# Optimization experiments

Hardware: AMD Instinct MI355X
Metric: run time of the kernel (lower is better)

The kernel has to match this reference:

```python
import jax, jax.numpy as jnp
import numpy as np

EMB = 768
HEADS = 12
DEPTH = EMB // HEADS
B, L = 8, 1024


def setup_inputs() -> dict:
    key = jax.random.key(0)
    ks = jax.random.split(key, 11)
    s = 1.0 / np.sqrt(EMB)
    inp = {
        "v": jax.random.normal(ks[0], (B, L, EMB), jnp.float32),
        "k": jax.random.normal(ks[1], (B, L, EMB), jnp.float32),
        "q": jax.random.normal(ks[2], (B, L, EMB), jnp.float32),
        # torch Linear weights: [out_features, in_features]
        "wq_w": jax.random.normal(ks[3], (EMB, EMB), jnp.float32) * s,
        "wq_b": jax.random.normal(ks[4], (EMB,), jnp.float32) * s,
        "wk_w": jax.random.normal(ks[5], (EMB, EMB), jnp.float32) * s,
        "wk_b": jax.random.normal(ks[6], (EMB,), jnp.float32) * s,
        "wv_w": jax.random.normal(ks[7], (EMB, EMB), jnp.float32) * s,
        "wv_b": jax.random.normal(ks[8], (EMB,), jnp.float32) * s,
        "dense_w": jax.random.normal(ks[9], (EMB, EMB), jnp.float32) * s,
        "dense_b": jax.random.normal(ks[10], (EMB,), jnp.float32) * s,
    }
    return inp


def _split_heads(x):
    b, l, _ = x.shape
    return x.reshape(b, l, HEADS, DEPTH).transpose(0, 2, 1, 3)  # [b,h,l,d]


def reference(v, k, q, wq_w, wq_b, wk_w, wk_b, wv_w, wv_b, dense_w, dense_b):
    qh = _split_heads(q @ wq_w.T + wq_b)
    kh = _split_heads(k @ wk_w.T + wk_b)
    vh = _split_heads(v @ wv_w.T + wv_b)
    # NOTE: module scales by sqrt(embedding_dim), not sqrt(depth)
    scale = 1.0 / jnp.sqrt(jnp.asarray(EMB, qh.dtype))
    score = jnp.einsum("bhqd,bhkd->bhqk", qh, kh) * scale
    attn_w = jax.nn.softmax(score, axis=-1)  # [b,h,lq,lk]
    logits = jnp.einsum("bhqk,bhkd->bhqd", attn_w, vh)
    concat = logits.transpose(0, 2, 1, 3).reshape(q.shape[0], -1, EMB)
    attention = concat @ dense_w.T + dense_b  # dropout p=0 -> identity
    return attention, attn_w
```

## Files before the change

### kernel.cpp

```cpp
#include <hip/hip_runtime.h>

#define EMB 768
#define NH 12
#define HD 64
#define BBATCH 8
#define LL 1024
#define BL (BBATCH * LL)

typedef __attribute__((ext_vector_type(8))) short bf16x8;
typedef __attribute__((ext_vector_type(4))) float f32x4;

__device__ __forceinline__ unsigned int f2bfu(float f) {
  unsigned int u = __builtin_bit_cast(unsigned int, f);
  return (u + 0x7FFFu + ((u >> 16) & 1u)) >> 16;
}

__device__ __forceinline__ f32x4 mfma16(bf16x8 a, bf16x8 b, f32x4 c) {
  return __builtin_amdgcn_mfma_f32_16x16x32_bf16(a, b, c, 0, 0, 0);
}

__global__ __launch_bounds__(256) void convert_w_kernel(
    const float* __restrict__ wq, const float* __restrict__ wk,
    const float* __restrict__ wv, const float* __restrict__ wd,
    unsigned short* __restrict__ out) {
  const int n = EMB * EMB;
  int e = (blockIdx.x * 256 + threadIdx.x) * 4;
  int which = e / n;
  int off = e - which * n;
  const float* src = (which == 0) ? wq : (which == 1) ? wk : (which == 2) ? wv : wd;
  float4 v4 = *reinterpret_cast<const float4*>(src + off);
  uint2 o;
  o.x = f2bfu(v4.x) | (f2bfu(v4.y) << 16);
  o.y = f2bfu(v4.z) | (f2bfu(v4.w) << 16);
  *reinterpret_cast<uint2*>(out + e) = o;
}

template <int MODE>
__global__ __launch_bounds__(256) void gemm_xwt_kernel(
    const void* __restrict__ Xv, const unsigned short* __restrict__ W,
    const float* __restrict__ bias, void* __restrict__ outp, float out_scale) {
  constexpr bool IN_F32 = (MODE != 2);
  extern __shared__ char smem[];
  unsigned short* Ab = reinterpret_cast<unsigned short*>(smem);
  unsigned short* Bb = Ab + 128 * 32;

  const int t = threadIdx.x;
  const int lane = t & 63, wid = t >> 6;
  const int wr = wid >> 1, wc = wid & 1;
  const int lrow = lane & 15, lgrp = lane >> 4;
  const int bm0 = blockIdx.x * 128, bn0 = blockIdx.y * 128;

  f32x4 acc[4][4];
#pragma unroll
  for (int i = 0; i < 4; ++i)
#pragma unroll
    for (int j = 0; j < 4; ++j) acc[i][j] = (f32x4){0.f, 0.f, 0.f, 0.f};

  float4 aF[2][2];
  uint4 aB[2];
  uint4 bB[2];

  const int ar = t >> 2, as = t & 3;
  const int rb = t >> 1, sb = (t & 1) * 2;

  auto load_regs = [&](int kt) {
    const int k0 = kt * 32;
    if constexpr (IN_F32) {
      const float* X = reinterpret_cast<const float*>(Xv);
      const float* g0 = X + (size_t)(bm0 + ar) * EMB + k0 + as * 8;
      aF[0][0] = reinterpret_cast<const float4*>(g0)[0];
      aF[0][1] = reinterpret_cast<const float4*>(g0)[1];
      const float* g1 = g0 + (size_t)64 * EMB;
      aF[1][0] = reinterpret_cast<const float4*>(g1)[0];
      aF[1][1] = reinterpret_cast<const float4*>(g1)[1];
    } else {
      const unsigned short* X = reinterpret_cast<const unsigned short*>(Xv);
      const uint4* g = reinterpret_cast<const uint4*>(X + (size_t)(bm0 + rb) * EMB + k0 + sb * 8);
      aB[0] = g[0];
      aB[1] = g[1];
    }
    const uint4* gw = reinterpret_cast<const uint4*>(W + (size_t)(bn0 + rb) * EMB + k0 + sb * 8);
    bB[0] = gw[0];
    bB[1] = gw[1];
  };

  auto write_lds = [&]() {
    if constexpr (IN_F32) {
#pragma unroll
      for (int it = 0; it < 2; ++it) {
        int r = ar + it * 64;
        uint4 pk;
        pk.x = f2bfu(aF[it][0].x) | (f2bfu(aF[it][0].y) << 16);
        pk.y = f2bfu(aF[it][0].z) | (f2bfu(aF[it][0].w) << 16);
        pk.z = f2bfu(aF[it][1].x) | (f2bfu(aF[it][1].y) << 16);
        pk.w = f2bfu(aF[it][1].z) | (f2bfu(aF[it][1].w) << 16);
        *reinterpret_cast<uint4*>(Ab + r * 32 + ((as ^ (r & 3)) * 8)) = pk;
      }
    } else {
      *reinterpret_cast<uint4*>(Ab + rb * 32 + ((sb ^ (rb & 3)) * 8)) = aB[0];
      *reinterpret_cast<uint4*>(Ab + rb * 32 + (((sb + 1) ^ (rb & 3)) * 8)) = aB[1];
    }
    *reinterpret_cast<uint4*>(Bb + rb * 32 + ((sb ^ (rb & 3)) * 8)) = bB[0];
    *reinterpret_cast<uint4*>(Bb + rb * 32 + (((sb + 1) ^ (rb & 3)) * 8)) = bB[1];
  };

  auto compute = [&]() {
    bf16x8 a[4], b[4];
    const int sw = (lgrp ^ (lrow & 3)) * 8;
#pragma unroll
    for (int i = 0; i < 4; ++i) {
      int r = wr * 64 + i * 16 + lrow;
      a[i] = *reinterpret_cast<const bf16x8*>(Ab + r * 32 + sw);
      int c = wc * 64 + i * 16 + lrow;
      b[i] = *reinterpret_cast<const bf16x8*>(Bb + c * 32 + sw);
    }
#pragma unroll
    for (int i = 0; i < 4; ++i)
#pragma unroll
      for (int j = 0; j < 4; ++j) acc[i][j] = mfma16(a[i], b[j], acc[i][j]);
  };

  load_regs(0);
  write_lds();
  __syncthreads();
#pragma unroll 1
  for (int kt = 0; kt < 24; ++kt) {
    if (kt < 23) load_regs(kt + 1);
    compute();
    __syncthreads();
    if (kt < 23) {
      write_lds();
      __syncthreads();
    }
  }

  if constexpr (MODE == 0) {
    unsigned short* out = reinterpret_cast<unsigned short*>(outp);
#pragma unroll
    for (int jj = 0; jj < 4; ++jj) {
      int C = bn0 + wc * 64 + jj * 16 + lrow;
      float bv = bias[C];
      int hh = C >> 6, dd = C & 63;
#pragma unroll
      for (int i = 0; i < 4; ++i)
#pragma unroll
        for (int j2 = 0; j2 < 4; ++j2) {
          int R = bm0 + wr * 64 + i * 16 + lgrp * 4 + j2;
          int bidx = R >> 10, l = R & 1023;
          out[(((size_t)(bidx * NH + hh) * 1024 + l) << 6) + dd] =
              (unsigned short)f2bfu((acc[i][jj][j2] + bv) * out_scale);
        }
    }
  }

  if constexpr (MODE == 1) {
    __syncthreads();
    unsigned short* T = reinterpret_cast<unsigned short*>(smem);
#pragma unroll
    for (int jj = 0; jj < 4; ++jj) {
      int cl = wc * 64 + jj * 16 + lrow;
      float bv = bias[bn0 + cl];
#pragma unroll
      for (int i = 0; i < 4; ++i)
#pragma unroll
        for (int j2 = 0; j2 < 4; ++j2) {
          int rl = wr * 64 + i * 16 + lgrp * 4 + j2;
          T[cl * 136 + rl] = (unsigned short)f2bfu(acc[i][jj][j2] + bv);
        }
    }
    __syncthreads();
    unsigned short* out = reinterpret_cast<unsigned short*>(outp);
    int cl = t >> 1, rh = (t & 1) * 64;
    int C = bn0 + cl, hh = C >> 6, dd = C & 63;
    int Rg = bm0 + rh, bidx = Rg >> 10, l0 = Rg & 1023;
    size_t obase = ((size_t)(bidx * NH + hh) * 64 + dd) * 1024 + l0;
#pragma unroll
    for (int q8 = 0; q8 < 8; ++q8) {
      uint4 val = *reinterpret_cast<const uint4*>(T + cl * 136 + rh + q8 * 8);
      *reinterpret_cast<uint4*>(out + obase + q8 * 8) = val;
    }
  }

  if constexpr (MODE == 2) {
    float* out = reinterpret_cast<float*>(outp);
#pragma unroll
    for (int jj = 0; jj < 4; ++jj) {
      int C = bn0 + wc * 64 + jj * 16 + lrow;
      float bv = bias[C];
#pragma unroll
      for (int i = 0; i < 4; ++i)
#pragma unroll
        for (int j2 = 0; j2 < 4; ++j2) {
          int R = bm0 + wr * 64 + i * 16 + lgrp * 4 + j2;
          out[(size_t)R * EMB + C] = acc[i][jj][j2] + bv;
        }
    }
  }
}

__global__ __launch_bounds__(256) void attn_kernel(
    const unsigned short* __restrict__ qh, const unsigned short* __restrict__ kh,
    const unsigned short* __restrict__ vhT, float* __restrict__ attn_w,
    unsigned short* __restrict__ concat) {
  __shared__ unsigned short Pl[16 * 1024];
  __shared__ float red[2][4][16];

  const int t = threadIdx.x;
  const int lane = t & 63, w = t >> 6;
  const int lrow = lane & 15, lgrp = lane >> 4;
  const int qt = blockIdx.x, pair = blockIdx.y;
  const int b = pair / NH, h = pair - b * NH;
  const int q0 = qt * 16;
  const unsigned short* qbase = qh + (size_t)pair * (LL * HD);
  const unsigned short* kbase = kh + (size_t)pair * (LL * HD);
  const unsigned short* vbase = vhT + (size_t)pair * (HD * LL);

  bf16x8 aq[2];
#pragma unroll
  for (int c = 0; c < 2; ++c)
    aq[c] = *reinterpret_cast<const bf16x8*>(qbase + (size_t)(q0 + lrow) * HD + c * 32 + lgrp * 8);

  f32x4 acc[16];
#pragma unroll
  for (int f = 0; f < 16; ++f) acc[f] = (f32x4){0.f, 0.f, 0.f, 0.f};

  const int k0 = w * 256;
#pragma unroll
  for (int f = 0; f < 16; ++f) {
    const unsigned short* kr = kbase + (size_t)(k0 + f * 16 + lrow) * HD + lgrp * 8;
    bf16x8 b0 = *reinterpret_cast<const bf16x8*>(kr);
    bf16x8 b1 = *reinterpret_cast<const bf16x8*>(kr + 32);
    acc[f] = mfma16(aq[0], b0, acc[f]);
    acc[f] = mfma16(aq[1], b1, acc[f]);
  }

  float m0[4], s0[4];
#pragma unroll
  for (int j = 0; j < 4; ++j) m0[j] = acc[0][j];
#pragma unroll
  for (int f = 1; f < 16; ++f)
#pragma unroll
    for (int j = 0; j < 4; ++j) m0[j] = fmaxf(m0[j], acc[f][j]);
#pragma unroll
  for (int mask = 1; mask < 16; mask <<= 1)
#pragma unroll
    for (int j = 0; j < 4; ++j) m0[j] = fmaxf(m0[j], __shfl_xor(m0[j], mask));
  if ((lane & 15) == 0) {
#pragma unroll
    for (int j = 0; j < 4; ++j) red[0][w][lgrp * 4 + j] = m0[j];
  }
  __syncthreads();
  float M[4];
#pragma unroll
  for (int j = 0; j < 4; ++j) {
    int r = lgrp * 4 + j;
    M[j] = fmaxf(fmaxf(red[0][0][r], red[0][1][r]), fmaxf(red[0][2][r], red[0][3][r]));
    s0[j] = 0.f;
  }
#pragma unroll
  for (int f = 0; f < 16; ++f)
#pragma unroll
    for (int j = 0; j < 4; ++j) {
      float p = __expf(acc[f][j] - M[j]);
      acc[f][j] = p;
      s0[j] += p;
    }
#pragma unroll
  for (int mask = 1; mask < 16; mask <<= 1)
#pragma unroll
    for (int j = 0; j < 4; ++j) s0[j] += __shfl_xor(s0[j], mask);
  if ((lane & 15) == 0) {
#pragma unroll
    for (int j = 0; j < 4; ++j) red[1][w][lgrp * 4 + j] = s0[j];
  }
  __syncthreads();
  float inv[4];
#pragma unroll
  for (int j = 0; j < 4; ++j) {
    int r = lgrp * 4 + j;
    inv[j] = 1.0f / (red[1][0][r] + red[1][1][r] + red[1][2][r] + red[1][3][r]);
  }

  float* awp = attn_w + (size_t)pair * (LL * LL);
#pragma unroll
  for (int f = 0; f < 16; ++f) {
    int col = k0 + f * 16 + lrow;
#pragma unroll
    for (int j = 0; j < 4; ++j) {
      int prow = lgrp * 4 + j;
      float v = acc[f][j] * inv[j];
      __builtin_nontemporal_store(v, awp + (size_t)(q0 + prow) * LL + col);
      int byte = (prow * 2048 + col * 2) ^ ((prow & 7) << 4);
      *reinterpret_cast<unsigned short*>(reinterpret_cast<char*>(Pl) + byte) =
          (unsigned short)f2bfu(v);
    }
  }
  __syncthreads();

  f32x4 o = (f32x4){0.f, 0.f, 0.f, 0.f};
  const unsigned short* vrow = vbase + (size_t)(w * 16 + lrow) * LL;
#pragma unroll
  for (int kk = 0; kk < 32; ++kk) {
    int byte = (lrow * 2048 + (kk * 32 + lgrp * 8) * 2) ^ ((lrow & 7) << 4);
    bf16x8 pa = *reinterpret_cast<const bf16x8*>(reinterpret_cast<char*>(Pl) + byte);
    bf16x8 vb = *reinterpret_cast<const bf16x8*>(vrow + kk * 32 + lgrp * 8);
    o = mfma16(pa, vb, o);
  }
#pragma unroll
  for (int j = 0; j < 4; ++j) {
    int row = q0 + lgrp * 4 + j;
    int cc = h * 64 + w * 16 + lrow;
    concat[((size_t)b * LL + row) * EMB + cc] = (unsigned short)f2bfu(o[j]);
  }
}

extern "C" void kernel_launch(void* const* d_in, const int* in_sizes, int n_in,
                              void* d_out, int out_size, void* d_ws, size_t ws_size,
                              hipStream_t stream) {
  const float* v = (const float*)d_in[0];
  const float* k = (const float*)d_in[1];
  const float* q = (const float*)d_in[2];
  const float* wq_w = (const float*)d_in[3];
  const float* wq_b = (const float*)d_in[4];
  const float* wk_w = (const float*)d_in[5];
  const float* wk_b = (const float*)d_in[6];
  const float* wv_w = (const float*)d_in[7];
  const float* wv_b = (const float*)d_in[8];
  const float* dw = (const float*)d_in[9];
  const float* db = (const float*)d_in[10];

  float* out_attn = (float*)d_out;
  float* out_w = out_attn + (size_t)BL * EMB;

  if (ws_size < 55050240u) return;
  unsigned short* ws = (unsigned short*)d_ws;
  unsigned short* wqb16 = ws;
  unsigned short* wkb16 = wqb16 + EMB * EMB;
  unsigned short* wvb16 = wkb16 + EMB * EMB;
  unsigned short* wdb16 = wvb16 + EMB * EMB;
  unsigned short* qhb = wdb16 + EMB * EMB;
  unsigned short* khb = qhb + (size_t)BL * EMB;
  unsigned short* vtb = khb + (size_t)BL * EMB;
  unsigned short* cat = vtb + (size_t)BL * EMB;

  convert_w_kernel<<<dim3(2304), dim3(256), 0, stream>>>(wq_w, wk_w, wv_w, dw, ws);

  const float scale = 0.036084391824351615f;
  dim3 gg(64, 6);
  gemm_xwt_kernel<0><<<gg, 256, 16384, stream>>>(q, wqb16, wq_b, qhb, scale);
  gemm_xwt_kernel<0><<<gg, 256, 16384, stream>>>(k, wkb16, wk_b, khb, 1.0f);
  gemm_xwt_kernel<1><<<gg, 256, 128 * 136 * 2, stream>>>(v, wvb16, wv_b, vtb, 1.0f);

  attn_kernel<<<dim3(64, 96), 256, 0, stream>>>(qhb, khb, vtb, out_w, cat);

  gemm_xwt_kernel<2><<<gg, 256, 16384, stream>>>(cat, wdb16, db, out_attn, 1.0f);
}
```

Before: 390.9 us.

## Fuse QKV projections into one launch, double-buffer GEMM LDS, vectorize epilogues

The three Q/K/V projection GEMMs now run as a single grid-z launch. The GEMM core double-buffers its LDS tiles so there is one barrier per k-step, and swaps MFMA operands so each lane writes four contiguous output columns as vector stores. The attention kernel likewise swaps MFMA operands so softmax rows map to lanes, which cuts shuffle reductions and enables float4 nontemporal stores of attention weights. It also prefetches part of V and adds setprio hints around the MFMA loops. Larger LDS use and launch_bounds occupancy hints may change register pressure.

```diff
diff --git a/kernel.cpp b/kernel.cpp
--- a/kernel.cpp
+++ b/kernel.cpp
@@ -35,31 +35,20 @@
   *reinterpret_cast<uint2*>(out + e) = o;
 }
 
-template <int MODE>
-__global__ __launch_bounds__(256) void gemm_xwt_kernel(
-    const void* __restrict__ Xv, const unsigned short* __restrict__ W,
-    const float* __restrict__ bias, void* __restrict__ outp, float out_scale) {
-  constexpr bool IN_F32 = (MODE != 2);
-  extern __shared__ char smem[];
-  unsigned short* Ab = reinterpret_cast<unsigned short*>(smem);
-  unsigned short* Bb = Ab + 128 * 32;
-
+template <bool IN_F32>
+__device__ __forceinline__ void gemm_core(const void* __restrict__ Xv,
+                                          const unsigned short* __restrict__ W,
+                                          char* smem, f32x4 (&acc)[4][4],
+                                          int bm0, int bn0) {
+  unsigned short* S = reinterpret_cast<unsigned short*>(smem);
   const int t = threadIdx.x;
-  const int lane = t & 63, wid = t >> 6;
+  const int lane = t & 63;
+  const int wid = t >> 6;
   const int wr = wid >> 1, wc = wid & 1;
   const int lrow = lane & 15, lgrp = lane >> 4;
-  const int bm0 = blockIdx.x * 128, bn0 = blockIdx.y * 128;
-
-  f32x4 acc[4][4];
-#pragma unroll
-  for (int i = 0; i < 4; ++i)
-#pragma unroll
-    for (int j = 0; j < 4; ++j) acc[i][j] = (f32x4){0.f, 0.f, 0.f, 0.f};
 
   float4 aF[2][2];
-  uint4 aB[2];
-  uint4 bB[2];
-
+  uint4 aB[2], bB[2];
   const int ar = t >> 2, as = t & 3;
   const int rb = t >> 1, sb = (t & 1) * 2;
 
@@ -84,7 +73,9 @@
     bB[1] = gw[1];
   };
 
-  auto write_lds = [&]() {
+  auto write_lds = [&](int buf) {
+    unsigned short* Ab = S + buf * 8192;
+    unsigned short* Bb = Ab + 4096;
     if constexpr (IN_F32) {
 #pragma unroll
       for (int it = 0; it < 2; ++it) {
@@ -104,72 +95,101 @@
     *reinterpret_cast<uint4*>(Bb + rb * 32 + (((sb + 1) ^ (rb & 3)) * 8)) = bB[1];
   };
 
-  auto compute = [&]() {
+  auto compute = [&](int buf) {
+    unsigned short* Ab = S + buf * 8192;
+    unsigned short* Bb = Ab + 4096;
     bf16x8 a[4], b[4];
     const int sw = (lgrp ^ (lrow & 3)) * 8;
 #pragma unroll
     for (int i = 0; i < 4; ++i) {
-      int r = wr * 64 + i * 16 + lrow;
-      a[i] = *reinterpret_cast<const bf16x8*>(Ab + r * 32 + sw);
-      int c = wc * 64 + i * 16 + lrow;
-      b[i] = *reinterpret_cast<const bf16x8*>(Bb + c * 32 + sw);
-    }
+      a[i] = *reinterpret_cast<const bf16x8*>(Ab + (wr * 64 + i * 16 + lrow) * 32 + sw);
+      b[i] = *reinterpret_cast<const bf16x8*>(Bb + (wc * 64 + i * 16 + lrow) * 32 + sw);
+    }
+    __builtin_amdgcn_s_setprio(1);
 #pragma unroll
     for (int i = 0; i < 4; ++i)
 #pragma unroll
-      for (int j = 0; j < 4; ++j) acc[i][j] = mfma16(a[i], b[j], acc[i][j]);
+      for (int j = 0; j < 4; ++j) acc[i][j] = mfma16(b[i], a[j], acc[i][j]);
+    __builtin_amdgcn_s_setprio(0);
   };
 
   load_regs(0);
-  write_lds();
+  write_lds(0);
   __syncthreads();
 #pragma unroll 1
   for (int kt = 0; kt < 24; ++kt) {
+    int cur = kt & 1;
     if (kt < 23) load_regs(kt + 1);
-    compute();
+    compute(cur);
+    if (kt < 23) write_lds(cur ^ 1);
     __syncthreads();
-    if (kt < 23) {
-      write_lds();
-      __syncthreads();
-    }
-  }
-
-  if constexpr (MODE == 0) {
-    unsigned short* out = reinterpret_cast<unsigned short*>(outp);
-#pragma unroll
-    for (int jj = 0; jj < 4; ++jj) {
-      int C = bn0 + wc * 64 + jj * 16 + lrow;
-      float bv = bias[C];
-      int hh = C >> 6, dd = C & 63;
-#pragma unroll
-      for (int i = 0; i < 4; ++i)
-#pragma unroll
-        for (int j2 = 0; j2 < 4; ++j2) {
-          int R = bm0 + wr * 64 + i * 16 + lgrp * 4 + j2;
-          int bidx = R >> 10, l = R & 1023;
-          out[(((size_t)(bidx * NH + hh) * 1024 + l) << 6) + dd] =
-              (unsigned short)f2bfu((acc[i][jj][j2] + bv) * out_scale);
-        }
-    }
-  }
-
-  if constexpr (MODE == 1) {
+  }
+}
+
+__global__ __launch_bounds__(256, 4) void qkv_kernel(
+    const float* __restrict__ qin, const float* __restrict__ kin, const float* __restrict__ vin,
+    const unsigned short* __restrict__ wq, const unsigned short* __restrict__ wk,
+    const unsigned short* __restrict__ wv, const float* __restrict__ bq,
+    const float* __restrict__ bk, const float* __restrict__ bv,
+    unsigned short* __restrict__ qh, unsigned short* __restrict__ kh,
+    unsigned short* __restrict__ vT) {
+  extern __shared__ char smem[];
+  const int z = blockIdx.z;
+  const float* X = (z == 0) ? qin : (z == 1) ? kin : vin;
+  const unsigned short* W = (z == 0) ? wq : (z == 1) ? wk : wv;
+  const float* bias = (z == 0) ? bq : (z == 1) ? bk : bv;
+  const int bm0 = blockIdx.x * 128, bn0 = blockIdx.y * 128;
+
+  f32x4 acc[4][4];
+#pragma unroll
+  for (int i = 0; i < 4; ++i)
+#pragma unroll
+    for (int j = 0; j < 4; ++j) acc[i][j] = (f32x4){0.f, 0.f, 0.f, 0.f};
+
+  gemm_core<true>(X, W, smem, acc, bm0, bn0);
+
+  const int t = threadIdx.x;
+  const int lane = t & 63, wid = t >> 6;
+  const int wr = wid >> 1, wc = wid & 1;
+  const int lrow = lane & 15, lgrp = lane >> 4;
+
+  if (z < 2) {
+    const float out_scale = (z == 0) ? 0.036084391824351615f : 1.0f;
+    unsigned short* out = (z == 0) ? qh : kh;
+#pragma unroll
+    for (int i = 0; i < 4; ++i) {
+      int c0 = bn0 + wc * 64 + i * 16 + lgrp * 4;
+      float4 bv4 = *reinterpret_cast<const float4*>(bias + c0);
+      int hh = c0 >> 6, dd0 = c0 & 63;
+#pragma unroll
+      for (int j = 0; j < 4; ++j) {
+        int R = bm0 + wr * 64 + j * 16 + lrow;
+        int bidx = R >> 10, l = R & 1023;
+        uint2 o;
+        o.x = f2bfu((acc[i][j][0] + bv4.x) * out_scale) |
+              (f2bfu((acc[i][j][1] + bv4.y) * out_scale) << 16);
+        o.y = f2bfu((acc[i][j][2] + bv4.z) * out_scale) |
+              (f2bfu((acc[i][j][3] + bv4.w) * out_scale) << 16);
+        *reinterpret_cast<uint2*>(out + (((size_t)(bidx * NH + hh)) << 16) + (l << 6) + dd0) = o;
+      }
+    }
+  } else {
     __syncthreads();
     unsigned short* T = reinterpret_cast<unsigned short*>(smem);
 #pragma unroll
-    for (int jj = 0; jj < 4; ++jj) {
-      int cl = wc * 64 + jj * 16 + lrow;
-      float bv = bias[bn0 + cl];
-#pragma unroll
-      for (int i = 0; i < 4; ++i)
-#pragma unroll
-        for (int j2 = 0; j2 < 4; ++j2) {
-          int rl = wr * 64 + i * 16 + lgrp * 4 + j2;
-          T[cl * 136 + rl] = (unsigned short)f2bfu(acc[i][jj][j2] + bv);
-        }
+    for (int i = 0; i < 4; ++i) {
+      int c0 = wc * 64 + i * 16 + lgrp * 4;
+      float4 bv4 = *reinterpret_cast<const float4*>(bias + bn0 + c0);
+#pragma unroll
+      for (int j = 0; j < 4; ++j) {
+        int rl = wr * 64 + j * 16 + lrow;
+        T[(c0 + 0) * 136 + rl] = (unsigned short)f2bfu(acc[i][j][0] + bv4.x);
+        T[(c0 + 1) * 136 + rl] = (unsigned short)f2bfu(acc[i][j][1] + bv4.y);
+        T[(c0 + 2) * 136 + rl] = (unsigned short)f2bfu(acc[i][j][2] + bv4.z);
+        T[(c0 + 3) * 136 + rl] = (unsigned short)f2bfu(acc[i][j][3] + bv4.w);
+      }
     }
     __syncthreads();
-    unsigned short* out = reinterpret_cast<unsigned short*>(outp);
     int cl = t >> 1, rh = (t & 1) * 64;
     int C = bn0 + cl, hh = C >> 6, dd = C & 63;
     int Rg = bm0 + rh, bidx = Rg >> 10, l0 = Rg & 1023;
@@ -177,28 +197,46 @@
 #pragma unroll
     for (int q8 = 0; q8 < 8; ++q8) {
       uint4 val = *reinterpret_cast<const uint4*>(T + cl * 136 + rh + q8 * 8);
-      *reinterpret_cast<uint4*>(out + obase + q8 * 8) = val;
-    }
-  }
-
-  if constexpr (MODE == 2) {
-    float* out = reinterpret_cast<float*>(outp);
-#pragma unroll
-    for (int jj = 0; jj < 4; ++jj) {
-      int C = bn0 + wc * 64 + jj * 16 + lrow;
-      float bv = bias[C];
-#pragma unroll
-      for (int i = 0; i < 4; ++i)
-#pragma unroll
-        for (int j2 = 0; j2 < 4; ++j2) {
-          int R = bm0 + wr * 64 + i * 16 + lgrp * 4 + j2;
-          out[(size_t)R * EMB + C] = acc[i][jj][j2] + bv;
-        }
-    }
-  }
-}
-
-__global__ __launch_bounds__(256) void attn_kernel(
+      *reinterpret_cast<uint4*>(vT + obase + q8 * 8) = val;
+    }
+  }
+}
+
+__global__ __launch_bounds__(256, 4) void dense_kernel(
+    const unsigned short* __restrict__ X, const unsigned short* __restrict__ W,
+    const float* __restrict__ bias, float* __restrict__ out) {
+  extern __shared__ char smem[];
+  const int bm0 = blockIdx.x * 128, bn0 = blockIdx.y * 128;
+  f32x4 acc[4][4];
+#pragma unroll
+  for (int i = 0; i < 4; ++i)
+#pragma unroll
+    for (int j = 0; j < 4; ++j) acc[i][j] = (f32x4){0.f, 0.f, 0.f, 0.f};
+
+  gemm_core<false>(X, W, smem, acc, bm0, bn0);
+
+  const int t = threadIdx.x;
+  const int lane = t & 63, wid = t >> 6;
+  const int wr = wid >> 1, wc = wid & 1;
+  const int lrow = lane & 15, lgrp = lane >> 4;
+#pragma unroll
+  for (int i = 0; i < 4; ++i) {
+    int c0 = bn0 + wc * 64 + i * 16 + lgrp * 4;
+    float4 bv4 = *reinterpret_cast<const float4*>(bias + c0);
+#pragma unroll
+    for (int j = 0; j < 4; ++j) {
+      int R = bm0 + wr * 64 + j * 16 + lrow;
+      f32x4 o;
+      o[0] = acc[i][j][0] + bv4.x;
+      o[1] = acc[i][j][1] + bv4.y;
+      o[2] = acc[i][j][2] + bv4.z;
+      o[3] = acc[i][j][3] + bv4.w;
+      *reinterpret_cast<f32x4*>(out + (size_t)R * EMB + c0) = o;
+    }
+  }
+}
+
+__global__ __launch_bounds__(256, 4) void attn_kernel(
     const unsigned short* __restrict__ qh, const unsigned short* __restrict__ kh,
     const unsigned short* __restrict__ vhT, float* __restrict__ attn_w,
     unsigned short* __restrict__ concat) {
@@ -225,87 +263,76 @@
   for (int f = 0; f < 16; ++f) acc[f] = (f32x4){0.f, 0.f, 0.f, 0.f};
 
   const int k0 = w * 256;
+  __builtin_amdgcn_s_setprio(1);
 #pragma unroll
   for (int f = 0; f < 16; ++f) {
     const unsigned short* kr = kbase + (size_t)(k0 + f * 16 + lrow) * HD + lgrp * 8;
     bf16x8 b0 = *reinterpret_cast<const bf16x8*>(kr);
     bf16x8 b1 = *reinterpret_cast<const bf16x8*>(kr + 32);
-    acc[f] = mfma16(aq[0], b0, acc[f]);
-    acc[f] = mfma16(aq[1], b1, acc[f]);
-  }
-
-  float m0[4], s0[4];
-#pragma unroll
-  for (int j = 0; j < 4; ++j) m0[j] = acc[0][j];
-#pragma unroll
-  for (int f = 1; f < 16; ++f)
-#pragma unroll
-    for (int j = 0; j < 4; ++j) m0[j] = fmaxf(m0[j], acc[f][j]);
-#pragma unroll
-  for (int mask = 1; mask < 16; mask <<= 1)
-#pragma unroll
-    for (int j = 0; j < 4; ++j) m0[j] = fmaxf(m0[j], __shfl_xor(m0[j], mask));
-  if ((lane & 15) == 0) {
-#pragma unroll
-    for (int j = 0; j < 4; ++j) red[0][w][lgrp * 4 + j] = m0[j];
-  }
+    acc[f] = mfma16(b0, aq[0], acc[f]);
+    acc[f] = mfma16(b1, aq[1], acc[f]);
+  }
+  __builtin_amdgcn_s_setprio(0);
+
+  const unsigned short* vrow = vbase + (size_t)(w * 16 + lrow) * LL;
+  bf16x8 vpre[8];
+#pragma unroll
+  for (int kk = 0; kk < 8; ++kk)
+    vpre[kk] = *reinterpret_cast<const bf16x8*>(vrow + kk * 32 + lgrp * 8);
+
+  float m = acc[0][0];
+#pragma unroll
+  for (int f = 0; f < 16; ++f)
+#pragma unroll
+    for (int j = 0; j < 4; ++j) m = fmaxf(m, acc[f][j]);
+  m = fmaxf(m, __shfl_xor(m, 16));
+  m = fmaxf(m, __shfl_xor(m, 32));
+  if (lane < 16) red[0][w][lane] = m;
   __syncthreads();
-  float M[4];
-#pragma unroll
-  for (int j = 0; j < 4; ++j) {
-    int r = lgrp * 4 + j;
-    M[j] = fmaxf(fmaxf(red[0][0][r], red[0][1][r]), fmaxf(red[0][2][r], red[0][3][r]));
-    s0[j] = 0.f;
-  }
+  float M = fmaxf(fmaxf(red[0][0][lrow], red[0][1][lrow]),
+                  fmaxf(red[0][2][lrow], red[0][3][lrow]));
+  float s = 0.f;
 #pragma unroll
   for (int f = 0; f < 16; ++f)
 #pragma unroll
     for (int j = 0; j < 4; ++j) {
-      float p = __expf(acc[f][j] - M[j]);
+      float p = __expf(acc[f][j] - M);
       acc[f][j] = p;
-      s0[j] += p;
-    }
-#pragma unroll
-  for (int mask = 1; mask < 16; mask <<= 1)
-#pragma unroll
-    for (int j = 0; j < 4; ++j) s0[j] += __shfl_xor(s0[j], mask);
-  if ((lane & 15) == 0) {
-#pragma unroll
-    for (int j = 0; j < 4; ++j) red[1][w][lgrp * 4 + j] = s0[j];
-  }
+      s += p;
+    }
+  s += __shfl_xor(s, 16);
+  s += __shfl_xor(s, 32);
+  if (lane < 16) red[1][w][lane] = s;
   __syncthreads();
-  float inv[4];
-#pragma unroll
-  for (int j = 0; j < 4; ++j) {
-    int r = lgrp * 4 + j;
-    inv[j] = 1.0f / (red[1][0][r] + red[1][1][r] + red[1][2][r] + red[1][3][r]);
-  }
-
-  float* awp = attn_w + (size_t)pair * (LL * LL);
+  float inv = 1.0f / (red[1][0][lrow] + red[1][1][lrow] + red[1][2][lrow] + red[1][3][lrow]);
+
+  float* awp = attn_w + (size_t)pair * (LL * LL) + (size_t)(q0 + lrow) * LL + k0 + lgrp * 4;
+  char* Plb = reinterpret_cast<char*>(Pl);
 #pragma unroll
   for (int f = 0; f < 16; ++f) {
-    int col = k0 + f * 16 + lrow;
-#pragma unroll
-    for (int j = 0; j < 4; ++j) {
-      int prow = lgrp * 4 + j;
-      float v = acc[f][j] * inv[j];
-      __builtin_nontemporal_store(v, awp + (size_t)(q0 + prow) * LL + col);
-      int byte = (prow * 2048 + col * 2) ^ ((prow & 7) << 4);
-      *reinterpret_cast<unsigned short*>(reinterpret_cast<char*>(Pl) + byte) =
-          (unsigned short)f2bfu(v);
-    }
+    float p0 = acc[f][0] * inv, p1 = acc[f][1] * inv;
+    float p2 = acc[f][2] * inv, p3 = acc[f][3] * inv;
+    f32x4 o = {p0, p1, p2, p3};
+    __builtin_nontemporal_store(o, reinterpret_cast<f32x4*>(awp + f * 16));
+    uint2 pb;
+    pb.x = f2bfu(p0) | (f2bfu(p1) << 16);
+    pb.y = f2bfu(p2) | (f2bfu(p3) << 16);
+    int byte = (lrow * 2048 + (k0 + f * 16 + lgrp * 4) * 2) ^ ((lrow & 7) << 4);
+    *reinterpret_cast<uint2*>(Plb + byte) = pb;
   }
   __syncthreads();
 
   f32x4 o = (f32x4){0.f, 0.f, 0.f, 0.f};
-  const unsigned short* vrow = vbase + (size_t)(w * 16 + lrow) * LL;
+  __builtin_amdgcn_s_setprio(1);
 #pragma unroll
   for (int kk = 0; kk < 32; ++kk) {
     int byte = (lrow * 2048 + (kk * 32 + lgrp * 8) * 2) ^ ((lrow & 7) << 4);
-    bf16x8 pa = *reinterpret_cast<const bf16x8*>(reinterpret_cast<char*>(Pl) + byte);
-    bf16x8 vb = *reinterpret_cast<const bf16x8*>(vrow + kk * 32 + lgrp * 8);
+    bf16x8 pa = *reinterpret_cast<const bf16x8*>(Plb + byte);
+    bf16x8 vb = (kk < 8) ? vpre[kk]
+                         : *reinterpret_cast<const bf16x8*>(vrow + kk * 32 + lgrp * 8);
     o = mfma16(pa, vb, o);
   }
+  __builtin_amdgcn_s_setprio(0);
 #pragma unroll
   for (int j = 0; j < 4; ++j) {
     int row = q0 + lgrp * 4 + j;
@@ -345,13 +372,10 @@
 
   convert_w_kernel<<<dim3(2304), dim3(256), 0, stream>>>(wq_w, wk_w, wv_w, dw, ws);
 
-  const float scale = 0.036084391824351615f;
-  dim3 gg(64, 6);
-  gemm_xwt_kernel<0><<<gg, 256, 16384, stream>>>(q, wqb16, wq_b, qhb, scale);
-  gemm_xwt_kernel<0><<<gg, 256, 16384, stream>>>(k, wkb16, wk_b, khb, 1.0f);
-  gemm_xwt_kernel<1><<<gg, 256, 128 * 136 * 2, stream>>>(v, wvb16, wv_b, vtb, 1.0f);
-
-  attn_kernel<<<dim3(64, 96), 256, 0, stream>>>(qhb, khb, vtb, out_w, cat);
-
-  gemm_xwt_kernel<2><<<gg, 256, 16384, stream>>>(cat, wdb16, db, out_attn, 1.0f);
-}
+  qkv_kernel<<<dim3(64, 6, 3), dim3(256), 34816, stream>>>(
+      q, k, v, wqb16, wkb16, wvb16, wq_b, wk_b, wv_b, qhb, khb, vtb);
+
+  attn_kernel<<<dim3(64, 96), dim3(256), 0, stream>>>(qhb, khb, vtb, out_w, cat);
+
+  dense_kernel<<<dim3(64, 6), dim3(256), 32768, stream>>>(cat, wdb16, db, out_attn);
+}
```

After: 522.5 us. +33.7%, slower.
